# Performance work log

Measured on AMD Instinct MI355X. Metric: run time of the kernel, lower is better.

Reference implementation:

```python
import jax, jax.numpy as jnp
import numpy as np

NEG_SLOPE = 0.2
EPS = 1e-16


def gat_conv(x, src, dst, W, att_src, att_dst, bias, heads, out_ch):
    """PyG-style GATConv. src/dst already include self-loops. Messages flow src -> dst."""
    N = x.shape[0]
    h = (x @ W).reshape(N, heads, out_ch)          # [N, H, C]
    a_src = jnp.sum(h * att_src, axis=-1)          # [N, H]
    a_dst = jnp.sum(h * att_dst, axis=-1)          # [N, H]
    e = a_src[src] + a_dst[dst]                    # [E, H]
    e = jax.nn.leaky_relu(e, NEG_SLOPE)
    # softmax over incoming edges per destination node
    m = jax.ops.segment_max(e, dst, num_segments=N)      # [N, H]
    m = jnp.where(jnp.isfinite(m), m, 0.0)
    ex = jnp.exp(e - m[dst])                       # [E, H]
    denom = jax.ops.segment_sum(ex, dst, num_segments=N)  # [N, H]
    alpha = ex / (denom[dst] + EPS)                # [E, H]
    msg = alpha[:, :, None] * h[src]               # [E, H, C]
    out = jax.ops.segment_sum(msg, dst, num_segments=N)   # [N, H, C]
    return out, bias


def add_self_loops(edge_index, N):
    loop = jnp.arange(N, dtype=edge_index.dtype)
    src = jnp.concatenate([edge_index[0], loop])
    dst = jnp.concatenate([edge_index[1], loop])
    return src, dst


def setup_inputs() -> dict:
    key = jax.random.key(0)
    ks = jax.random.split(key, 10)
    N, E, IN, HID, OUT, H = 100000, 1600000, 128, 32, 32, 4
    s = lambda fan: 1.0 / np.sqrt(fan)
    return {
        "x": jax.random.normal(ks[0], (N, IN), dtype=jnp.float32),
        "edge_index": jax.random.randint(ks[1], (2, E), 0, N, dtype=jnp.int32),
        "W1": jax.random.normal(ks[2], (IN, H * HID), dtype=jnp.float32) * s(IN),
        "att_src1": jax.random.normal(ks[3], (H, HID), dtype=jnp.float32) * s(HID),
        "att_dst1": jax.random.normal(ks[4], (H, HID), dtype=jnp.float32) * s(HID),
        "b1": jnp.zeros((H * HID,), dtype=jnp.float32),
        "W2": jax.random.normal(ks[5], (H * HID, OUT), dtype=jnp.float32) * s(H * HID),
        "att_src2": jax.random.normal(ks[6], (1, OUT), dtype=jnp.float32) * s(OUT),
        "att_dst2": jax.random.normal(ks[7], (1, OUT), dtype=jnp.float32) * s(OUT),
        "b2": jnp.zeros((OUT,), dtype=jnp.float32),
    }


def reference(x, edge_index, W1, att_src1, att_dst1, b1, W2, att_src2, att_dst2, b2):
    N = x.shape[0]
    src, dst = add_self_loops(edge_index, N)
    # layer 1: 4 heads, concat=True
    out1, bias1 = gat_conv(x, src, dst, W1, att_src1, att_dst1, b1, heads=4, out_ch=32)
    h1 = jax.nn.relu(out1.reshape(N, -1) + bias1)          # [N, 128]
    # layer 2: 1 head, concat=False (mean over 1 head == squeeze)
    out2, bias2 = gat_conv(h1, src, dst, W2, att_src2, att_dst2, b2, heads=1, out_ch=32)
    return out2.mean(axis=1) + bias2                       # [N, 32]
```

## Files before the change

### kernel.cpp

```cpp
#include <hip/hip_runtime.h>
#include <hip/hip_bf16.h>


typedef __bf16 bf16x8 __attribute__((ext_vector_type(8)));
typedef float f32x4 __attribute__((ext_vector_type(4)));

__device__ __forceinline__ float lrelu(float v) { return v >= 0.f ? v : 0.2f * v; }

__device__ __forceinline__ unsigned f2bf(float f) {
    unsigned u = __float_as_uint(f);
    return (u + 0x7FFFu + ((u >> 16) & 1u)) >> 16;
}

__device__ __forceinline__ bf16x8 as_bf16x8(uint4 u) {
    union { uint4 u; bf16x8 b; } c; c.u = u; return c.b;
}

__device__ __forceinline__ void bf16x8_fma(uint4 hv, float a, float* acc) {
    acc[0] = fmaf(a, __uint_as_float(hv.x << 16), acc[0]);
    acc[1] = fmaf(a, __uint_as_float(hv.x & 0xFFFF0000u), acc[1]);
    acc[2] = fmaf(a, __uint_as_float(hv.y << 16), acc[2]);
    acc[3] = fmaf(a, __uint_as_float(hv.y & 0xFFFF0000u), acc[3]);
    acc[4] = fmaf(a, __uint_as_float(hv.z << 16), acc[4]);
    acc[5] = fmaf(a, __uint_as_float(hv.z & 0xFFFF0000u), acc[5]);
    acc[6] = fmaf(a, __uint_as_float(hv.w << 16), acc[6]);
    acc[7] = fmaf(a, __uint_as_float(hv.w & 0xFFFF0000u), acc[7]);
}

__global__ __launch_bounds__(256) void cast_w_k(const float* __restrict__ W1,
                                                const float* __restrict__ W2,
                                                ushort* __restrict__ w1t,
                                                ushort* __restrict__ w2t) {
    int tid = blockIdx.x * 256 + threadIdx.x;
    if (tid < 16384) {
        int k = tid >> 7, c = tid & 127;
        w1t[c * 128 + k] = (ushort)f2bf(W1[tid]);
    }
    if (tid < 4096) {
        int k = tid >> 5, c = tid & 31;
        w2t[c * 128 + k] = (ushort)f2bf(W2[tid]);
    }
}

__global__ __launch_bounds__(256) void gemm1_hist_k(
    const float* __restrict__ x, const ushort* __restrict__ w1t,
    const float* __restrict__ atts, const float* __restrict__ attd,
    ushort* __restrict__ h, float* __restrict__ as_, float* __restrict__ ad_,
    const int* __restrict__ ei, int* __restrict__ deg, int* __restrict__ rank,
    int N, int E, int nbG) {
    if (blockIdx.x >= nbG) {
        int e = (blockIdx.x - nbG) * 256 + threadIdx.x;
        if (e < E + N) {
            int d = (e < E) ? ei[E + e] : e - E;
            rank[e] = atomicAdd(&deg[d], 1);
        }
        return;
    }
    const int w = threadIdx.x >> 6;
    const int l = threadIdx.x & 63;
    const int c15 = l & 15;
    const int quad = l >> 4;
    const int n_base = blockIdx.x * 64 + w * 16;
    const int n = n_base + c15;

    bf16x8 a[4];
    if (n < N) {
        const float4* xr = (const float4*)(x + (size_t)n * 128);
#pragma unroll
        for (int ks = 0; ks < 4; ks++) {
            float4 p0 = xr[ks * 8 + quad * 2];
            float4 p1 = xr[ks * 8 + quad * 2 + 1];
            uint4 u;
            u.x = f2bf(p0.x) | (f2bf(p0.y) << 16);
            u.y = f2bf(p0.z) | (f2bf(p0.w) << 16);
            u.z = f2bf(p1.x) | (f2bf(p1.y) << 16);
            u.w = f2bf(p1.z) | (f2bf(p1.w) << 16);
            a[ks] = as_bf16x8(u);
        }
    } else {
        uint4 z = make_uint4(0, 0, 0, 0);
#pragma unroll
        for (int ks = 0; ks < 4; ks++) a[ks] = as_bf16x8(z);
    }

    f32x4 acc[8];
#pragma unroll
    for (int ct = 0; ct < 8; ct++) acc[ct] = (f32x4){0.f, 0.f, 0.f, 0.f};

#pragma unroll
    for (int ct = 0; ct < 8; ct++) {
        const uint4* wr = (const uint4*)(w1t + (size_t)(ct * 16 + c15) * 128);
#pragma unroll
        for (int ks = 0; ks < 4; ks++) {
            bf16x8 bfrag = as_bf16x8(wr[ks * 4 + quad]);
            acc[ct] = __builtin_amdgcn_mfma_f32_16x16x32_bf16(a[ks], bfrag, acc[ct], 0, 0, 0);
        }
    }

#pragma unroll
    for (int ct = 0; ct < 8; ct++) {
        int col = ct * 16 + c15;
#pragma unroll
        for (int reg = 0; reg < 4; reg++) {
            int n_out = n_base + quad * 4 + reg;
            if (n_out < N) h[(size_t)n_out * 128 + col] = (ushort)f2bf(acc[ct][reg]);
        }
    }
#pragma unroll
    for (int hh = 0; hh < 4; hh++) {
        float sA = atts[hh * 32 + c15], sB = atts[hh * 32 + 16 + c15];
        float dA = attd[hh * 32 + c15], dB = attd[hh * 32 + 16 + c15];
#pragma unroll
        for (int reg = 0; reg < 4; reg++) {
            float ps = acc[2 * hh][reg] * sA + acc[2 * hh + 1][reg] * sB;
            float pd = acc[2 * hh][reg] * dA + acc[2 * hh + 1][reg] * dB;
            ps += __shfl_xor(ps, 1); pd += __shfl_xor(pd, 1);
            ps += __shfl_xor(ps, 2); pd += __shfl_xor(pd, 2);
            ps += __shfl_xor(ps, 4); pd += __shfl_xor(pd, 4);
            ps += __shfl_xor(ps, 8); pd += __shfl_xor(pd, 8);
            int n_out = n_base + quad * 4 + reg;
            if (c15 == 0 && n_out < N) { as_[n_out * 4 + hh] = ps; ad_[n_out * 4 + hh] = pd; }
        }
    }
}

__global__ __launch_bounds__(256) void scan1_k(const int* __restrict__ deg,
                                               int* __restrict__ tmp, int* __restrict__ partial, int N) {
    __shared__ int sh[256];
    int i = blockIdx.x * 256 + threadIdx.x;
    int v = (i < N) ? deg[i] : 0;
    sh[threadIdx.x] = v;
    __syncthreads();
#pragma unroll
    for (int off = 1; off < 256; off <<= 1) {
        int t = (threadIdx.x >= off) ? sh[threadIdx.x - off] : 0;
        __syncthreads();
        sh[threadIdx.x] += t;
        __syncthreads();
    }
    if (i < N) tmp[i] = sh[threadIdx.x];
    if (threadIdx.x == 255) partial[blockIdx.x] = sh[255];
}

__global__ __launch_bounds__(1024) void scan2_k(int* __restrict__ partial, int B) {
    __shared__ int sh[1024];
    int i = threadIdx.x;
    int v = (i < B) ? partial[i] : 0;
    sh[i] = v;
    __syncthreads();
#pragma unroll
    for (int off = 1; off < 1024; off <<= 1) {
        int t = (i >= off) ? sh[i - off] : 0;
        __syncthreads();
        sh[i] += t;
        __syncthreads();
    }
    if (i < B) partial[i] = sh[i] - v;
}

__global__ __launch_bounds__(256) void scan3_k(const int* __restrict__ tmp, const int* __restrict__ partial,
                                               int* __restrict__ rs, int N) {
    int i = blockIdx.x * 256 + threadIdx.x;
    if (i < N) rs[i + 1] = tmp[i] + partial[blockIdx.x];
    if (i == 0) rs[0] = 0;
}

__global__ __launch_bounds__(256) void scatter_k(const int* __restrict__ ei, const int* __restrict__ rank,
                                                 const int* __restrict__ rs, int E, int N,
                                                 int* __restrict__ csr) {
    int e = blockIdx.x * 256 + threadIdx.x;
    if (e >= E + N) return;
    int s, d;
    if (e < E) { s = ei[e]; d = ei[E + e]; } else { s = e - E; d = s; }
    csr[rs[d] + rank[e]] = s;
}

__global__ __launch_bounds__(256) void gather1_k(
    const int* __restrict__ rs, const int* __restrict__ csr,
    const float* __restrict__ as_, const float* __restrict__ ad_,
    const uint4* __restrict__ h, const float* __restrict__ b,
    const ushort* __restrict__ w2t, const float* __restrict__ atts2,
    const float* __restrict__ attd2,
    ushort* __restrict__ h2, float* __restrict__ as2, float* __restrict__ ad2,
    int N) {
    __shared__ uint4 o1s[16][18];
    const int jj = threadIdx.x & 31;
    const int l16 = jj & 15;
    const int sub = jj & 16;
    const int dl = (threadIdx.x >> 5) * 2 + (jj >> 4);
    const int d = blockIdx.x * 16 + dl;
    const int hl = l16 >> 2;
    const int sl = l16 & 3;
    int beg = 0, end = 0;
    float adv = 0.f;
    if (d < N) { beg = rs[d]; end = rs[d + 1]; adv = ad_[d * 4 + hl]; }

    float acc[8];
#pragma unroll
    for (int i = 0; i < 8; i++) acc[i] = 0.f;
    float den = 0.f;

    int j0 = beg;
    int sv0 = 0, sv1 = 0;
    float ex0 = 0.f, ex1 = 0.f;
    bool have = (j0 + 8 <= end);
    if (have) {
        sv0 = csr[j0 + sl];
        sv1 = csr[j0 + sl + 4];
        ex0 = __expf(fminf(lrelu(as_[sv0 * 4 + hl] + adv), 80.f));
        ex1 = __expf(fminf(lrelu(as_[sv1 * 4 + hl] + adv), 80.f));
    }
    while (have) {
        bool nhave = (j0 + 16 <= end);
        int na = nhave ? (j0 + 8) : beg;
        int psv0 = csr[na + sl];
        int psv1 = csr[na + sl + 4];
        den += ex0 + ex1;
        float av[8]; uint4 hv[8];
#pragma unroll
        for (int e = 0; e < 8; e++) {
            const int k = e >> 2, q = e & 3;
            const int srcl = sub + (l16 & 12) + q;
            float exk = k ? ex1 : ex0;
            int   svk = k ? sv1 : sv0;
            av[e] = __shfl(exk, srcl, 32);
            int s = __shfl(svk, srcl, 32);
            hv[e] = h[(size_t)s * 16 + l16];
        }
        float pex0 = __expf(fminf(lrelu(as_[psv0 * 4 + hl] + adv), 80.f));
        float pex1 = __expf(fminf(lrelu(as_[psv1 * 4 + hl] + adv), 80.f));
#pragma unroll
        for (int e = 0; e < 8; e++) bf16x8_fma(hv[e], av[e], acc);
        sv0 = psv0; sv1 = psv1; ex0 = pex0; ex1 = pex1;
        j0 += 8; have = nhave;
    }
    int r = end - j0;
    if (r > 0) {
        float ex0r = 0.f, ex1r = 0.f;
        int   sv0r = 0,   sv1r = 0;
        if (sl < r) {
            sv0r = csr[j0 + sl];
            ex0r = __expf(fminf(lrelu(as_[sv0r * 4 + hl] + adv), 80.f));
            den += ex0r;
        }
        if (sl + 4 < r) {
            sv1r = csr[j0 + sl + 4];
            ex1r = __expf(fminf(lrelu(as_[sv1r * 4 + hl] + adv), 80.f));
            den += ex1r;
        }
        float av[8]; uint4 hv[8];
#pragma unroll
        for (int e = 0; e < 8; e++) {
            const int k = e >> 2, q = e & 3;
            const int srcl = sub + (l16 & 12) + q;
            float exk = k ? ex1r : ex0r;
            int   svk = k ? sv1r : sv0r;
            av[e] = __shfl(exk, srcl, 32);
            int s = __shfl(svk, srcl, 32);
            if (e < r) hv[e] = h[(size_t)s * 16 + l16];
        }
#pragma unroll
        for (int e = 0; e < 8; e++) if (e < r) bf16x8_fma(hv[e], av[e], acc);
    }
    den += __shfl_xor(den, 1, 32);
    den += __shfl_xor(den, 2, 32);
    const float rcp = 1.f / (den + 1e-16f);
    float4 b0 = *(const float4*)&b[l16 * 8];
    float4 b1 = *(const float4*)&b[l16 * 8 + 4];
    float v0 = fmaxf(acc[0] * rcp + b0.x, 0.f);
    float v1 = fmaxf(acc[1] * rcp + b0.y, 0.f);
    float v2 = fmaxf(acc[2] * rcp + b0.z, 0.f);
    float v3 = fmaxf(acc[3] * rcp + b0.w, 0.f);
    float v4 = fmaxf(acc[4] * rcp + b1.x, 0.f);
    float v5 = fmaxf(acc[5] * rcp + b1.y, 0.f);
    float v6 = fmaxf(acc[6] * rcp + b1.z, 0.f);
    float v7 = fmaxf(acc[7] * rcp + b1.w, 0.f);
    uint4 pk;
    pk.x = f2bf(v0) | (f2bf(v1) << 16);
    pk.y = f2bf(v2) | (f2bf(v3) << 16);
    pk.z = f2bf(v4) | (f2bf(v5) << 16);
    pk.w = f2bf(v6) | (f2bf(v7) << 16);
    o1s[dl][l16] = pk;
    __syncthreads();

    if (threadIdx.x < 64) {
        const int l = threadIdx.x;
        const int c15g = l & 15;
        const int quad = l >> 4;
        bf16x8 a2[4];
#pragma unroll
        for (int ks = 0; ks < 4; ks++) a2[ks] = as_bf16x8(o1s[c15g][ks * 4 + quad]);
        f32x4 acc2[2];
#pragma unroll
        for (int ct = 0; ct < 2; ct++) acc2[ct] = (f32x4){0.f, 0.f, 0.f, 0.f};
#pragma unroll
        for (int ct = 0; ct < 2; ct++) {
            const uint4* wr = (const uint4*)(w2t + (size_t)(ct * 16 + c15g) * 128);
#pragma unroll
            for (int ks = 0; ks < 4; ks++) {
                bf16x8 bfrag = as_bf16x8(wr[ks * 4 + quad]);
                acc2[ct] = __builtin_amdgcn_mfma_f32_16x16x32_bf16(a2[ks], bfrag, acc2[ct], 0, 0, 0);
            }
        }
        const int nb = blockIdx.x * 16;
#pragma unroll
        for (int ct = 0; ct < 2; ct++) {
            int col = ct * 16 + c15g;
#pragma unroll
            for (int reg = 0; reg < 4; reg++) {
                int n_out = nb + quad * 4 + reg;
                if (n_out < N) h2[(size_t)n_out * 32 + col] = (ushort)f2bf(acc2[ct][reg]);
            }
        }
        float sA = atts2[c15g], sB = atts2[16 + c15g];
        float dA = attd2[c15g], dB = attd2[16 + c15g];
#pragma unroll
        for (int reg = 0; reg < 4; reg++) {
            float ps = acc2[0][reg] * sA + acc2[1][reg] * sB;
            float pd = acc2[0][reg] * dA + acc2[1][reg] * dB;
            ps += __shfl_xor(ps, 1); pd += __shfl_xor(pd, 1);
            ps += __shfl_xor(ps, 2); pd += __shfl_xor(pd, 2);
            ps += __shfl_xor(ps, 4); pd += __shfl_xor(pd, 4);
            ps += __shfl_xor(ps, 8); pd += __shfl_xor(pd, 8);
            int n_out = nb + quad * 4 + reg;
            if (c15g == 0 && n_out < N) { as2[n_out] = ps; ad2[n_out] = pd; }
        }
    }
}

__global__ __launch_bounds__(256) void gather2_k(
    const int* __restrict__ rs, const int* __restrict__ csr,
    const float* __restrict__ as_, const float* __restrict__ ad_,
    const uint4* __restrict__ h, const float* __restrict__ b,
    float* __restrict__ o, int N) {
    const int jj = threadIdx.x & 31;
    const int l4 = jj & 3;
    const int sub = jj & 28;
    const int d = blockIdx.x * 64 + (threadIdx.x >> 5) * 8 + (jj >> 2);
    if (d >= N) return;
    const int beg = rs[d], end = rs[d + 1];
    const float adv = ad_[d];

    float acc[8];
#pragma unroll
    for (int i = 0; i < 8; i++) acc[i] = 0.f;
    float den = 0.f;

    int j0 = beg;
    int sv0 = 0, sv1 = 0;
    float ex0 = 0.f, ex1 = 0.f;
    bool have = (j0 + 8 <= end);
    if (have) {
        sv0 = csr[j0 + l4];
        sv1 = csr[j0 + l4 + 4];
        ex0 = __expf(fminf(lrelu(as_[sv0] + adv), 80.f));
        ex1 = __expf(fminf(lrelu(as_[sv1] + adv), 80.f));
    }
    while (have) {
        bool nhave = (j0 + 16 <= end);
        int na = nhave ? (j0 + 8) : beg;
        int psv0 = csr[na + l4];
        int psv1 = csr[na + l4 + 4];
        den += ex0 + ex1;
        float av[8]; uint4 hv[8];
#pragma unroll
        for (int e = 0; e < 8; e++) {
            const int k = e >> 2, q = e & 3;
            const int srcl = sub + q;
            float exk = k ? ex1 : ex0;
            int   svk = k ? sv1 : sv0;
            av[e] = __shfl(exk, srcl, 32);
            int s = __shfl(svk, srcl, 32);
            hv[e] = h[(size_t)s * 4 + l4];
        }
        float pex0 = __expf(fminf(lrelu(as_[psv0] + adv), 80.f));
        float pex1 = __expf(fminf(lrelu(as_[psv1] + adv), 80.f));
#pragma unroll
        for (int e = 0; e < 8; e++) bf16x8_fma(hv[e], av[e], acc);
        sv0 = psv0; sv1 = psv1; ex0 = pex0; ex1 = pex1;
        j0 += 8; have = nhave;
    }
    int r = end - j0;
    if (r > 0) {
        float ex0r = 0.f, ex1r = 0.f;
        int   sv0r = 0,   sv1r = 0;
        if (l4 < r) {
            sv0r = csr[j0 + l4];
            ex0r = __expf(fminf(lrelu(as_[sv0r] + adv), 80.f));
            den += ex0r;
        }
        if (l4 + 4 < r) {
            sv1r = csr[j0 + l4 + 4];
            ex1r = __expf(fminf(lrelu(as_[sv1r] + adv), 80.f));
            den += ex1r;
        }
        float av[8]; uint4 hv[8];
#pragma unroll
        for (int e = 0; e < 8; e++) {
            const int k = e >> 2, q = e & 3;
            const int srcl = sub + q;
            float exk = k ? ex1r : ex0r;
            int   svk = k ? sv1r : sv0r;
            av[e] = __shfl(exk, srcl, 32);
            int s = __shfl(svk, srcl, 32);
            if (e < r) hv[e] = h[(size_t)s * 4 + l4];
        }
#pragma unroll
        for (int e = 0; e < 8; e++) if (e < r) bf16x8_fma(hv[e], av[e], acc);
    }
    den += __shfl_xor(den, 1, 32);
    den += __shfl_xor(den, 2, 32);
    const float rcp = 1.f / (den + 1e-16f);
    float4 b0 = *(const float4*)&b[l4 * 8];
    float4 b1 = *(const float4*)&b[l4 * 8 + 4];
    float4 o0, o1v;
    o0.x  = acc[0] * rcp + b0.x;
    o0.y  = acc[1] * rcp + b0.y;
    o0.z  = acc[2] * rcp + b0.z;
    o0.w  = acc[3] * rcp + b0.w;
    o1v.x = acc[4] * rcp + b1.x;
    o1v.y = acc[5] * rcp + b1.y;
    o1v.z = acc[6] * rcp + b1.z;
    o1v.w = acc[7] * rcp + b1.w;
    *(float4*)&o[(size_t)d * 32 + l4 * 8]     = o0;
    *(float4*)&o[(size_t)d * 32 + l4 * 8 + 4] = o1v;
}

extern "C" void kernel_launch(void* const* d_in, const int* in_sizes, int n_in,
                              void* d_out, int out_size, void* d_ws, size_t ws_size,
                              hipStream_t stream) {
    const float* x    = (const float*)d_in[0];
    const int*   ei   = (const int*)d_in[1];
    const float* W1   = (const float*)d_in[2];
    const float* as1v = (const float*)d_in[3];
    const float* ad1v = (const float*)d_in[4];
    const float* b1   = (const float*)d_in[5];
    const float* W2   = (const float*)d_in[6];
    const float* as2v = (const float*)d_in[7];
    const float* ad2v = (const float*)d_in[8];
    const float* b2   = (const float*)d_in[9];
    float* out = (float*)d_out;

    const int N = in_sizes[0] / 128;
    const int E = in_sizes[1] / 2;
    const int EN = E + N;
    const int B = (N + 255) / 256;

    char* base = (char*)d_ws;
    size_t o = 0;
    auto alloc = [&](size_t bytes) { void* p = base + o; o += (bytes + 255) & ~(size_t)255; return p; };
    ushort* w1t  = (ushort*)alloc((size_t)128 * 128 * 2);
    ushort* w2t  = (ushort*)alloc((size_t)32 * 128 * 2);
    ushort* h1   = (ushort*)alloc((size_t)N * 128 * 2);
    ushort* h2   = (ushort*)alloc((size_t)N * 32 * 2);
    float*  as1  = (float*)alloc((size_t)N * 4 * 4);
    float*  ad1  = (float*)alloc((size_t)N * 4 * 4);
    float*  as2  = (float*)alloc((size_t)N * 4);
    float*  ad2  = (float*)alloc((size_t)N * 4);
    int*    deg  = (int*)alloc((size_t)N * 4);
    int*    tmp  = (int*)alloc((size_t)N * 4);
    int*    part = (int*)alloc((size_t)1024 * 4);
    int*    rs   = (int*)alloc((size_t)(N + 1) * 4);
    int*    rank = (int*)alloc((size_t)EN * 4);
    int*    csr  = (int*)alloc((size_t)EN * 4);

    hipMemsetAsync(deg, 0, (size_t)N * 4, stream);

    const int nbE = (EN + 255) / 256;
    const int nbN = (N + 255) / 256;
    const int nbG = (N + 63) / 64;

    cast_w_k<<<64, 256, 0, stream>>>(W1, W2, w1t, w2t);
    gemm1_hist_k<<<nbG + nbE, 256, 0, stream>>>(x, w1t, as1v, ad1v, h1, as1, ad1,
                                                ei, deg, rank, N, E, nbG);
    scan1_k<<<nbN, 256, 0, stream>>>(deg, tmp, part, N);
    scan2_k<<<1, 1024, 0, stream>>>(part, B);
    scan3_k<<<nbN, 256, 0, stream>>>(tmp, part, rs, N);
    scatter_k<<<nbE, 256, 0, stream>>>(ei, rank, rs, E, N, csr);

    gather1_k<<<(N + 15) / 16, 256, 0, stream>>>(rs, csr, as1, ad1, (const uint4*)h1, b1,
                                                 w2t, as2v, ad2v, h2, as2, ad2, N);

    gather2_k<<<(N + 63) / 64, 256, 0, stream>>>(rs, csr, as2, ad2, (const uint4*)h2, b2, out, N);
}
```

Measured before the change: 347.3 us.

## Split fused GEMM/histogram kernel and batch edges per thread in hist and scatter

The combined GEMM-plus-degree-histogram launch is split into a standalone MFMA GEMM kernel and a separate histogram/rank kernel. The new histogram kernel has each thread process 8 edges, loading destinations with int4 reads and storing ranks with int4 writes. The scatter kernel now handles 4 edges per thread. The goal is fewer threads and more memory-level parallelism per thread on the atomic-heavy passes, at the cost of an extra launch and losing the overlap between GEMM and histogram blocks.

```diff
diff --git a/kernel.cpp b/kernel.cpp
--- a/kernel.cpp
+++ b/kernel.cpp
@@ -42,20 +42,10 @@
     }
 }
 
-__global__ __launch_bounds__(256) void gemm1_hist_k(
+__global__ __launch_bounds__(256) void gemm1_mfma(
     const float* __restrict__ x, const ushort* __restrict__ w1t,
     const float* __restrict__ atts, const float* __restrict__ attd,
-    ushort* __restrict__ h, float* __restrict__ as_, float* __restrict__ ad_,
-    const int* __restrict__ ei, int* __restrict__ deg, int* __restrict__ rank,
-    int N, int E, int nbG) {
-    if (blockIdx.x >= nbG) {
-        int e = (blockIdx.x - nbG) * 256 + threadIdx.x;
-        if (e < E + N) {
-            int d = (e < E) ? ei[E + e] : e - E;
-            rank[e] = atomicAdd(&deg[d], 1);
-        }
-        return;
-    }
+    ushort* __restrict__ h, float* __restrict__ as_, float* __restrict__ ad_, int N) {
     const int w = threadIdx.x >> 6;
     const int l = threadIdx.x & 63;
     const int c15 = l & 15;
@@ -124,6 +114,39 @@
     }
 }
 
+__global__ __launch_bounds__(256) void hist_rank_k(const int* __restrict__ ei, int E, int N,
+                                                   int* __restrict__ deg, int* __restrict__ rank) {
+    const int EN = E + N;
+    const int base = (blockIdx.x * 256 + threadIdx.x) * 8;
+    if (base >= EN) return;
+    int dd[8];
+    if (base + 8 <= E) {
+        int4 a = *(const int4*)&ei[E + base];
+        int4 c = *(const int4*)&ei[E + base + 4];
+        dd[0] = a.x; dd[1] = a.y; dd[2] = a.z; dd[3] = a.w;
+        dd[4] = c.x; dd[5] = c.y; dd[6] = c.z; dd[7] = c.w;
+    } else {
+#pragma unroll
+        for (int k = 0; k < 8; k++) {
+            int e = base + k;
+            dd[k] = (e < EN) ? ((e < E) ? ei[E + e] : e - E) : 0;
+        }
+    }
+    int rr[8];
+#pragma unroll
+    for (int k = 0; k < 8; k++) {
+        int e = base + k;
+        if (e < EN) rr[k] = atomicAdd(&deg[dd[k]], 1);
+    }
+    if (base + 8 <= EN) {
+        *(int4*)&rank[base]     = make_int4(rr[0], rr[1], rr[2], rr[3]);
+        *(int4*)&rank[base + 4] = make_int4(rr[4], rr[5], rr[6], rr[7]);
+    } else {
+#pragma unroll
+        for (int k = 0; k < 8; k++) if (base + k < EN) rank[base + k] = rr[k];
+    }
+}
+
 __global__ __launch_bounds__(256) void scan1_k(const int* __restrict__ deg,
                                                int* __restrict__ tmp, int* __restrict__ partial, int N) {
     __shared__ int sh[256];
@@ -168,11 +191,18 @@
 __global__ __launch_bounds__(256) void scatter_k(const int* __restrict__ ei, const int* __restrict__ rank,
                                                  const int* __restrict__ rs, int E, int N,
                                                  int* __restrict__ csr) {
-    int e = blockIdx.x * 256 + threadIdx.x;
-    if (e >= E + N) return;
-    int s, d;
-    if (e < E) { s = ei[e]; d = ei[E + e]; } else { s = e - E; d = s; }
-    csr[rs[d] + rank[e]] = s;
+    const int EN = E + N;
+    const int base = (blockIdx.x * 256 + threadIdx.x) * 4;
+    if (base >= EN) return;
+#pragma unroll
+    for (int k = 0; k < 4; k++) {
+        int e = base + k;
+        if (e < EN) {
+            int s, d;
+            if (e < E) { s = ei[e]; d = ei[E + e]; } else { s = e - E; d = s; }
+            csr[rs[d] + rank[e]] = s;
+        }
+    }
 }
 
 __global__ __launch_bounds__(256) void gather1_k(
@@ -466,17 +496,18 @@
 
     hipMemsetAsync(deg, 0, (size_t)N * 4, stream);
 
-    const int nbE = (EN + 255) / 256;
+    const int nbE8 = ((EN + 7) / 8 + 255) / 256;
+    const int nbE4 = ((EN + 3) / 4 + 255) / 256;
     const int nbN = (N + 255) / 256;
     const int nbG = (N + 63) / 64;
 
     cast_w_k<<<64, 256, 0, stream>>>(W1, W2, w1t, w2t);
-    gemm1_hist_k<<<nbG + nbE, 256, 0, stream>>>(x, w1t, as1v, ad1v, h1, as1, ad1,
-                                                ei, deg, rank, N, E, nbG);
+    gemm1_mfma<<<nbG, 256, 0, stream>>>(x, w1t, as1v, ad1v, h1, as1, ad1, N);
+    hist_rank_k<<<nbE8, 256, 0, stream>>>(ei, E, N, deg, rank);
     scan1_k<<<nbN, 256, 0, stream>>>(deg, tmp, part, N);
     scan2_k<<<1, 1024, 0, stream>>>(part, B);
     scan3_k<<<nbN, 256, 0, stream>>>(tmp, part, rs, N);
-    scatter_k<<<nbE, 256, 0, stream>>>(ei, rank, rs, E, N, csr);
+    scatter_k<<<nbE4, 256, 0, stream>>>(ei, rank, rs, E, N, csr);
 
     gather1_k<<<(N + 15) / 16, 256, 0, stream>>>(rs, csr, as1, ad1, (const uint4*)h1, b1,
                                                  w2t, as2v, ad2v, h2, as2, ad2, N);
```

Result: slower. 357.1 us (+2.8%).
